# Kernel tuning notes

Hardware: AMD Instinct MI355X
Metric: run time of the kernel (lower is better)

## Reference

```python
import jax, jax.numpy as jnp
import numpy as np

D_MODEL = 1024
N_HEADS = 16
WINDOW = 256
S_DIM = 128
BATCH = 1
SEQ = 4096
EPS = 1e-5


def setup_inputs() -> dict:
    key = jax.random.key(0)
    ks = jax.random.split(key, 10)
    d, s = D_MODEL, S_DIM

    def w(k, shape, fan_in):
        return jax.random.normal(k, shape, jnp.float32) * (fan_in ** -0.5)

    return {
        "x": jax.random.normal(ks[0], (BATCH, SEQ, d), jnp.float32),
        "ln1_g": jnp.ones((d,), jnp.float32), "ln1_b": jnp.zeros((d,), jnp.float32),
        "ln2_g": jnp.ones((d,), jnp.float32), "ln2_b": jnp.zeros((d,), jnp.float32),
        "W_qkv": w(ks[1], (d, 3 * d), d),
        "W_O": w(ks[2], (d, d), d), "b_O": jnp.zeros((d,), jnp.float32),
        "W_ug": w(ks[3], (d, s + d), d), "b_ug": jnp.zeros((s + d,), jnp.float32),
        "B_w": w(ks[4], (d, s), d),
        "A": jax.random.uniform(ks[5], (s,), jnp.float32, -0.1, 0.1),
        "C_w": w(ks[6], (s, d), s),
        "mlp_W1": w(ks[7], (d, 4 * d), d), "mlp_b1": jnp.zeros((4 * d,), jnp.float32),
        "mlp_W2": w(ks[8], (4 * d, d), 4 * d), "mlp_b2": jnp.zeros((d,), jnp.float32),
    }


def _layernorm(x, g, b):
    mu = jnp.mean(x, -1, keepdims=True)
    var = jnp.mean((x - mu) ** 2, -1, keepdims=True)
    return (x - mu) * jax.lax.rsqrt(var + EPS) * g + b


def _windowed_attn(xn, W_qkv, W_O, b_O):
    # Exact windowed causal attention: key j allowed iff j <= i and i - j < WINDOW.
    # Implemented block-locally (chunk size C = WINDOW) so no O(T^2) mask/scores
    # are materialized, matching the SDPA band-mask math exactly.
    Bq, T, d = xn.shape
    H, Dh, C = N_HEADS, d // N_HEADS, WINDOW
    N = T // C  # SEQ must be a multiple of WINDOW
    qkv = xn @ W_qkv
    q, k, v = jnp.split(qkv, 3, axis=-1)

    def blk(t):
        return t.reshape(Bq, T, H, Dh).transpose(0, 2, 1, 3).reshape(Bq, H, N, C, Dh)

    Qb, Kb, Vb = blk(q), blk(k), blk(v)

    def win(t):  # prepend previous block (zeros for block 0) -> [B,H,N,2C,Dh]
        prev = jnp.concatenate([jnp.zeros_like(t[:, :, :1]), t[:, :, :-1]], axis=2)
        return jnp.concatenate([prev, t], axis=3)

    Kw, Vw = win(Kb), win(Vb)
    scores = jnp.einsum('bhncd,bhnkd->bhnck', Qb, Kw) / np.sqrt(Dh).astype(np.float32)
    qi = jnp.arange(C)[:, None]
    kk = jnp.arange(2 * C)[None, :]
    band = (kk > qi) & (kk <= qi + C)            # window band within 2C keys
    mask = jnp.where((jnp.arange(N) == 0)[:, None, None], band & (kk >= C), band)
    scores = jnp.where(mask[None, None], scores, -jnp.inf)
    p = jax.nn.softmax(scores, axis=-1)
    o = jnp.einsum('bhnck,bhnkd->bhncd', p, Vw)
    o = o.reshape(Bq, H, T, Dh).transpose(0, 2, 1, 3).reshape(Bq, T, d)
    return o @ W_O + b_O


def reference(x, ln1_g, ln1_b, ln2_g, ln2_b, W_qkv, W_O, b_O, W_ug, b_ug,
              B_w, A, C_w, mlp_W1, mlp_b1, mlp_W2, mlp_b2):
    xn = _layernorm(x, ln1_g, ln1_b)
    # local path: windowed causal attention (eval mode: dropout = identity)
    attn = _windowed_attn(xn, W_qkv, W_O, b_O)
    # global path: linear SSM  s_t = A * s_{t-1} + (B x_t + u_t),  y_t = C s_t
    ug = xn @ W_ug + b_ug
    u = ug[..., :S_DIM]
    g = jax.nn.sigmoid(ug[..., S_DIM:])          # learnable fusion gate, [B,T,d]
    drive = xn @ B_w + u                          # [B,T,S]

    def step(s, ut):
        s2 = A * s + ut
        return s2, s2

    s0 = jnp.zeros((x.shape[0], S_DIM), x.dtype)
    _, states = jax.lax.scan(step, s0, drive.transpose(1, 0, 2))  # [T,B,S]
    y_ssm = jnp.einsum('tbs,sd->btd', states, C_w)
    # gated fusion + residual
    x = x + g * attn + (1.0 - g) * y_ssm
    # MLP block (exact GELU, as nn.GELU default)
    h = _layernorm(x, ln2_g, ln2_b)
    x = x + jax.nn.gelu(h @ mlp_W1 + mlp_b1, approximate=False) @ mlp_W2 + mlp_b2
    return x
```

## Files before the change

### kernel.cpp

```cpp
#include <hip/hip_runtime.h>
#include <hip/hip_bf16.h>
#include <math.h>

typedef short bf16x8 __attribute__((ext_vector_type(8)));
typedef float f32x4  __attribute__((ext_vector_type(4)));

#define GLOBAL_AS __attribute__((address_space(1)))
#define LDS_AS    __attribute__((address_space(3)))

__device__ __forceinline__ void async16(const void* g, void* l) {
  __builtin_amdgcn_global_load_lds((GLOBAL_AS void*)(g), (LDS_AS void*)(l), 16, 0, 0);
}

__device__ __forceinline__ unsigned short f2bf(float f){
  union { float f; unsigned u; } x; x.f = f;
  return (unsigned short)((x.u + 0x7fffu + ((x.u >> 16) & 1u)) >> 16);
}
__device__ __forceinline__ float bf2f(short s){
  union { unsigned u; float f; } x; x.u = ((unsigned)(unsigned short)s) << 16;
  return x.f;
}
__device__ __forceinline__ float gelu_f(float x){
  return 0.5f*x*(1.f+erff(x*0.70710678118654752f));
}

__global__ __launch_bounds__(256) void ln_bf16(const float* __restrict__ in,
    const float* __restrict__ gg, const float* __restrict__ bb, short* __restrict__ out)
{
  const int row = blockIdx.x;
  const int tid = threadIdx.x;
  const float4 v = reinterpret_cast<const float4*>(in + (size_t)row*1024)[tid];
  float s  = v.x+v.y+v.z+v.w;
  float sq = v.x*v.x+v.y*v.y+v.z*v.z+v.w*v.w;
  #pragma unroll
  for (int off=32; off; off>>=1){ s += __shfl_xor(s,off); sq += __shfl_xor(sq,off); }
  __shared__ float ss[4], qs[4];
  const int wid = tid>>6, lane = tid&63;
  if (lane==0){ ss[wid]=s; qs[wid]=sq; }
  __syncthreads();
  s  = ss[0]+ss[1]+ss[2]+ss[3];
  sq = qs[0]+qs[1]+qs[2]+qs[3];
  const float mu  = s * (1.f/1024.f);
  const float var = sq*(1.f/1024.f) - mu*mu;
  const float rs  = rsqrtf(var + 1e-5f);
  const float4 g4 = reinterpret_cast<const float4*>(gg)[tid];
  const float4 b4 = reinterpret_cast<const float4*>(bb)[tid];
  ushort4 o;
  o.x = f2bf((v.x-mu)*rs*g4.x+b4.x);
  o.y = f2bf((v.y-mu)*rs*g4.y+b4.y);
  o.z = f2bf((v.z-mu)*rs*g4.z+b4.z);
  o.w = f2bf((v.w-mu)*rs*g4.w+b4.w);
  *reinterpret_cast<ushort4*>(out + (size_t)row*1024 + tid*4) = o;
}

__device__ __forceinline__ void conv_body(const float* __restrict__ in,
    short* __restrict__ out, int K, int N, const float* __restrict__ add, int addN,
    int bx, int by)
{
  __shared__ float tile[32][33];
  const int n0 = bx*32, k0 = by*32;
  const int r = threadIdx.x >> 3, c4 = (threadIdx.x & 7)*4;
  float4 v = *reinterpret_cast<const float4*>(&in[(size_t)(k0+r)*N + n0 + c4]);
  if (add && (n0 + c4) < addN) {
    const float* ap = &add[(size_t)(k0+r)*addN + n0 + c4];
    v.x += ap[0]; v.y += ap[1]; v.z += ap[2]; v.w += ap[3];
  }
  tile[r][c4+0]=v.x; tile[r][c4+1]=v.y; tile[r][c4+2]=v.z; tile[r][c4+3]=v.w;
  __syncthreads();
  ushort4 o;
  o.x = f2bf(tile[c4+0][r]); o.y = f2bf(tile[c4+1][r]);
  o.z = f2bf(tile[c4+2][r]); o.w = f2bf(tile[c4+3][r]);
  *reinterpret_cast<ushort4*>(&out[(size_t)(n0+r)*K + k0 + c4]) = o;
}

__global__ __launch_bounds__(256) void prep_weights(
    const float* __restrict__ W_qkv, const float* __restrict__ W_O,
    const float* __restrict__ W_ug,  const float* __restrict__ B_w,
    const float* __restrict__ C_w,   const float* __restrict__ W1,
    const float* __restrict__ W2,
    short* __restrict__ wT_qkv, short* __restrict__ wT_o,
    short* __restrict__ wT_ug,  short* __restrict__ wT_c,
    short* __restrict__ wT_1,   short* __restrict__ wT_2)
{
  const int bid = blockIdx.x;
  if (bid < 3072) {
    conv_body(W_qkv, wT_qkv, 1024, 3072, nullptr, 0, bid % 96, bid / 96);
  } else if (bid < 4224) {
    const int j = bid - 3072;
    conv_body(W_ug, wT_ug, 1024, 1152, B_w, 128, j % 36, j / 36);
  } else if (bid < 5248) {
    const int j = bid - 4224;
    conv_body(W_O, wT_o, 1024, 1024, nullptr, 0, j % 32, j / 32);
  } else if (bid < 5376) {
    const int j = bid - 5248;
    conv_body(C_w, wT_c, 128, 1024, nullptr, 0, j % 32, j / 32);
  } else if (bid < 9472) {
    const int j = bid - 5376;
    conv_body(W1, wT_1, 1024, 4096, nullptr, 0, j % 128, j / 128);
  } else {
    const int j = bid - 9472;
    conv_body(W2, wT_2, 4096, 1024, nullptr, 0, j % 32, j / 32);
  }
}

template<int EPI>
__global__ __launch_bounds__(512) void gemm256(
    const short* __restrict__ A, const short* __restrict__ Bt,
    const float* __restrict__ bias, short* __restrict__ Cout,
    int M, int N, int K)
{
  extern __shared__ char lds[];
  const int tid = threadIdx.x;
  const int ln = tid & 63, w = tid >> 6;
  const int wr = w >> 2, wc = w & 3;
  const int lane15 = ln & 15, lgrp = ln >> 4;

  const int gx = gridDim.x;
  const int nwg = gx * gridDim.y;
  int id = blockIdx.y * gx + blockIdx.x;
  if ((nwg & 7) == 0) { const int cpx = nwg >> 3; id = (id & 7) * cpx + (id >> 3); }
  const int m0 = (id / gx) * 256, n0 = (id % gx) * 256;

  const int NT = K >> 6;

  f32x4 acc[8][4];
  #pragma unroll
  for (int i=0;i<8;i++)
    #pragma unroll
    for (int j=0;j<4;j++) acc[i][j] = (f32x4){0.f,0.f,0.f,0.f};

  #define STG256(k0_, bufA_, bufB_, p_) { \
    const int slot = (p_)*512 + tid; \
    const int row = slot >> 3, blk = slot & 7; \
    const int sblk = blk ^ (row & 7); \
    async16(A  + (size_t)(m0+row)*K + (k0_) + sblk*8, (bufA_) + slot*16); \
    async16(Bt + (size_t)(n0+row)*K + (k0_) + sblk*8, (bufB_) + slot*16); }

  {
    char* bA = lds, *bB = lds + 32768;
    STG256(0, bA, bB, 0); STG256(0, bA, bB, 1); STG256(0, bA, bB, 2); STG256(0, bA, bB, 3);
    if (NT > 1) { char* cA = lds + 65536, *cB = cA + 32768; STG256(64, cA, cB, 0); }
    asm volatile("s_waitcnt vmcnt(0)" ::: "memory");
    __builtin_amdgcn_s_barrier();
    __builtin_amdgcn_sched_barrier(0);
  }

  for (int kt = 0; kt < NT; ++kt) {
    const int cur = kt & 1;
    char* rdA = lds + cur*65536;  char* rdB = rdA + 32768;
    char* wrA = lds + (cur^1)*65536; char* wrB = wrA + 32768;
    const int kn = (kt+1) << 6;
    bf16x8 bfr[4][2];
    #pragma unroll
    for (int ni = 0; ni < 4; ni++) {
      const int row = wc*64 + ni*16 + lane15;
      #pragma unroll
      for (int ks = 0; ks < 2; ks++) {
        const int b = (ks*4 + lgrp) ^ (row & 7);
        bfr[ni][ks] = *reinterpret_cast<const bf16x8*>(rdB + (row*8 + b)*16);
      }
    }
    if (kt+1 < NT) STG256(kn, wrA, wrB, 1);
    #pragma unroll
    for (int mq = 0; mq < 2; ++mq) {
      bf16x8 af[4][2];
      #pragma unroll
      for (int mi = 0; mi < 4; mi++) {
        const int row = wr*128 + (mq*4+mi)*16 + lane15;
        #pragma unroll
        for (int ks = 0; ks < 2; ks++) {
          const int b = (ks*4 + lgrp) ^ (row & 7);
          af[mi][ks] = *reinterpret_cast<const bf16x8*>(rdA + (row*8 + b)*16);
        }
      }
      if (kt+1 < NT) STG256(kn, wrA, wrB, 2+mq);
      #pragma unroll
      for (int mi = 0; mi < 4; mi++)
        #pragma unroll
        for (int ni = 0; ni < 4; ni++)
          #pragma unroll
          for (int ks = 0; ks < 2; ks++)
            acc[mq*4+mi][ni] = __builtin_amdgcn_mfma_f32_16x16x32_bf16(
                af[mi][ks], bfr[ni][ks], acc[mq*4+mi][ni], 0, 0, 0);
    }
    if (kt+1 < NT) {
      __builtin_amdgcn_s_barrier();
      if (kt+2 < NT) {
        STG256((kt+2) << 6, rdA, rdB, 0);
        asm volatile("s_waitcnt vmcnt(2)" ::: "memory");
      } else {
        asm volatile("s_waitcnt vmcnt(0)" ::: "memory");
      }
      __builtin_amdgcn_s_barrier();
      __builtin_amdgcn_sched_barrier(0);
    }
  }
  #undef STG256

  #pragma unroll
  for (int ni = 0; ni < 4; ni++) {
    const int col = n0 + wc*64 + ni*16 + lane15;
    const float bv = bias ? bias[col] : 0.f;
    #pragma unroll
    for (int mi = 0; mi < 8; mi++) {
      #pragma unroll
      for (int r = 0; r < 4; r++) {
        const int row = m0 + wr*128 + mi*16 + lgrp*4 + r;
        float v = acc[mi][ni][r] + bv;
        Cout[(size_t)row*N + col] = (short)f2bf(v);
      }
    }
  }
}

template<int MT, int EPI>
__global__ __launch_bounds__(256) void gemm128(
    const short* __restrict__ A, const short* __restrict__ Bt,
    const float* __restrict__ bias,
    short* __restrict__ e_g,
    void* __restrict__ Cout, int M, int N, int K)
{
  constexpr int BM  = MT * 32;
  constexpr int ABY = BM * 128;
  constexpr int STR = ABY + 16384;
  constexpr int MPQ = MT / 2;
  extern __shared__ char lds[];
  const int tid = threadIdx.x;
  const int ln = tid & 63, w = tid >> 6;
  const int wr = w >> 1, wc = w & 1;
  const int lane15 = ln & 15, lgrp = ln >> 4;

  const int gx = gridDim.x;
  const int nwg = gx * gridDim.y;
  int id = blockIdx.y * gx + blockIdx.x;
  if ((nwg & 7) == 0) { const int cpx = nwg >> 3; id = (id & 7) * cpx + (id >> 3); }
  const int m0 = (id / gx) * BM, n0 = (id % gx) * 128;

  const int NT = K >> 6;

  f32x4 acc[MT][4];
  #pragma unroll
  for (int i=0;i<MT;i++)
    #pragma unroll
    for (int j=0;j<4;j++) acc[i][j] = (f32x4){0.f,0.f,0.f,0.f};

  #define STG(k0_, bufA_, bufB_, p_) { \
    const int slot = (p_)*256 + tid; \
    const int row = slot >> 3, blk = slot & 7; \
    const int sblk = blk ^ (row & 7); \
    if ((p_) < MT) async16(A + (size_t)(m0+row)*K + (k0_) + sblk*8, (bufA_) + slot*16); \
    async16(Bt + (size_t)(n0+row)*K + (k0_) + sblk*8, (bufB_) + slot*16); }

  {
    char* bA = lds, *bB = lds + ABY;
    STG(0, bA, bB, 0); STG(0, bA, bB, 1); STG(0, bA, bB, 2); STG(0, bA, bB, 3);
    if (NT > 1) { char* cA = lds + STR, *cB = cA + ABY; STG(64, cA, cB, 0); }
    asm volatile("s_waitcnt vmcnt(0)" ::: "memory");
    __builtin_amdgcn_s_barrier();
    __builtin_amdgcn_sched_barrier(0);
  }

  for (int kt = 0; kt < NT; ++kt) {
    const int cur = kt & 1;
    char* rdA = lds + cur*STR;   char* rdB = rdA + ABY;
    char* wrA = lds + (cur^1)*STR; char* wrB = wrA + ABY;
    const int kn = (kt+1) << 6;
    bf16x8 bfr[4][2];
    #pragma unroll
    for (int ni = 0; ni < 4; ni++) {
      const int row = wc*64 + ni*16 + lane15;
      #pragma unroll
      for (int ks = 0; ks < 2; ks++) {
        const int b = (ks*4 + lgrp) ^ (row & 7);
        bfr[ni][ks] = *reinterpret_cast<const bf16x8*>(rdB + (row*8 + b)*16);
      }
    }
    if (kt+1 < NT) STG(kn, wrA, wrB, 1);
    #pragma unroll
    for (int mq = 0; mq < 2; ++mq) {
      bf16x8 af[MPQ][2];
      #pragma unroll
      for (int mi = 0; mi < MPQ; mi++) {
        const int row = wr*(MT*16) + (mq*MPQ+mi)*16 + lane15;
        #pragma unroll
        for (int ks = 0; ks < 2; ks++) {
          const int b = (ks*4 + lgrp) ^ (row & 7);
          af[mi][ks] = *reinterpret_cast<const bf16x8*>(rdA + (row*8 + b)*16);
        }
      }
      if (kt+1 < NT) STG(kn, wrA, wrB, 2+mq);
      #pragma unroll
      for (int mi = 0; mi < MPQ; mi++)
        #pragma unroll
        for (int ni = 0; ni < 4; ni++)
          #pragma unroll
          for (int ks = 0; ks < 2; ks++)
            acc[mq*MPQ+mi][ni] = __builtin_amdgcn_mfma_f32_16x16x32_bf16(
                af[mi][ks], bfr[ni][ks], acc[mq*MPQ+mi][ni], 0, 0, 0);
    }
    if (kt+1 < NT) {
      __builtin_amdgcn_s_barrier();
      if (kt+2 < NT) {
        STG((kt+2) << 6, rdA, rdB, 0);
        asm volatile("s_waitcnt vmcnt(2)" ::: "memory");
      } else {
        asm volatile("s_waitcnt vmcnt(0)" ::: "memory");
      }
      __builtin_amdgcn_s_barrier();
      __builtin_amdgcn_sched_barrier(0);
    }
  }
  #undef STG

  #pragma unroll
  for (int ni = 0; ni < 4; ni++) {
    const int col = n0 + wc*64 + ni*16 + lane15;
    const float bv = bias ? bias[col] : 0.f;
    #pragma unroll
    for (int mi = 0; mi < MT; mi++) {
      #pragma unroll
      for (int r = 0; r < 4; r++) {
        const int row = m0 + wr*(MT*16) + mi*16 + lgrp*4 + r;
        float v = acc[mi][ni][r] + bv;
        if (EPI == 1) {
          if (col < 128) ((float*)Cout)[(size_t)row*128 + col] = v;
          else {
            const float gs = 1.f/(1.f+__expf(-v));
            e_g[(size_t)row*1024 + col - 128] = (short)f2bf(gs);
          }
        } else if (EPI == 2) {
          ((short*)Cout)[(size_t)row*N + col] = (short)f2bf(gelu_f(v));
        } else {
          float* o = (float*)Cout;
          o[(size_t)row*N + col] = v + o[(size_t)row*N + col];
        }
      }
    }
  }
}

__global__ __launch_bounds__(256) void wo_comb(
    const short* __restrict__ A1, const short* __restrict__ B1t,
    const short* __restrict__ A2, const short* __restrict__ B2t,
    const float* __restrict__ bias, const float* __restrict__ e_x,
    const short* __restrict__ e_g, float* __restrict__ Cout)
{
  constexpr int ABY = 8192;
  constexpr int STR = ABY + 16384;
  extern __shared__ char lds[];
  const int tid = threadIdx.x;
  const int ln = tid & 63, w = tid >> 6;
  const int wr = w >> 1, wc = w & 1;
  const int lane15 = ln & 15, lgrp = ln >> 4;
  const int K = 1024, N = 1024;

  const int gx = gridDim.x;
  const int nwg = gx * gridDim.y;
  int id = blockIdx.y * gx + blockIdx.x;
  if ((nwg & 7) == 0) { const int cpx = nwg >> 3; id = (id & 7) * cpx + (id >> 3); }
  const int m0 = (id / gx) * 64, n0 = (id % gx) * 128;

  f32x4 acc1[2][4], acc2[2][4];
  #pragma unroll
  for (int i=0;i<2;i++)
    #pragma unroll
    for (int j=0;j<4;j++){ acc1[i][j] = (f32x4){0.f,0.f,0.f,0.f}; acc2[i][j] = (f32x4){0.f,0.f,0.f,0.f}; }

  #define STGW(Asrc_, Bsrc_, AK_, k0_, bufA_, bufB_, p_) { \
    const int slot = (p_)*256 + tid; \
    const int row = slot >> 3, blk = slot & 7; \
    const int sblk = blk ^ (row & 7); \
    if ((p_) < 2) async16(Asrc_ + (size_t)(m0+row)*(AK_) + (k0_) + sblk*8, (bufA_) + slot*16); \
    async16(Bsrc_ + (size_t)(n0+row)*(AK_) + (k0_) + sblk*8, (bufB_) + slot*16); }

  {
    char* bA = lds, *bB = lds + ABY;
    STGW(A1, B1t, K, 0, bA, bB, 0); STGW(A1, B1t, K, 0, bA, bB, 1);
    STGW(A1, B1t, K, 0, bA, bB, 2); STGW(A1, B1t, K, 0, bA, bB, 3);
    { char* cA = lds + STR, *cB = cA + ABY; STGW(A1, B1t, K, 64, cA, cB, 0); }
    asm volatile("s_waitcnt vmcnt(0)" ::: "memory");
    __builtin_amdgcn_s_barrier();
    __builtin_amdgcn_sched_barrier(0);
  }

  const int NT = 16;
  for (int kt = 0; kt < NT; ++kt) {
    const int cur = kt & 1;
    char* rdA = lds + cur*STR;   char* rdB = rdA + ABY;
    char* wrA = lds + (cur^1)*STR; char* wrB = wrA + ABY;
    const int kn = (kt+1) << 6;
    bf16x8 bfr[4][2];
    #pragma unroll
    for (int ni = 0; ni < 4; ni++) {
      const int row = wc*64 + ni*16 + lane15;
      #pragma unroll
      for (int ks = 0; ks < 2; ks++) {
        const int b = (ks*4 + lgrp) ^ (row & 7);
        bfr[ni][ks] = *reinterpret_cast<const bf16x8*>(rdB + (row*8 + b)*16);
      }
    }
    if (kt+1 < NT) STGW(A1, B1t, K, kn, wrA, wrB, 1);
    #pragma unroll
    for (int mq = 0; mq < 2; ++mq) {
      bf16x8 af[2];
      {
        const int row = wr*32 + mq*16 + lane15;
        #pragma unroll
        for (int ks = 0; ks < 2; ks++) {
          const int b = (ks*4 + lgrp) ^ (row & 7);
          af[ks] = *reinterpret_cast<const bf16x8*>(rdA + (row*8 + b)*16);
        }
      }
      if (kt+1 < NT) STGW(A1, B1t, K, kn, wrA, wrB, 2+mq);
      #pragma unroll
      for (int ni = 0; ni < 4; ni++)
        #pragma unroll
        for (int ks = 0; ks < 2; ks++)
          acc1[mq][ni] = __builtin_amdgcn_mfma_f32_16x16x32_bf16(
              af[ks], bfr[ni][ks], acc1[mq][ni], 0, 0, 0);
    }
    if (kt+1 < NT) {
      __builtin_amdgcn_s_barrier();
      if (kt+2 < NT) {
        STGW(A1, B1t, K, (kt+2) << 6, rdA, rdB, 0);
        asm volatile("s_waitcnt vmcnt(2)" ::: "memory");
      } else {
        asm volatile("s_waitcnt vmcnt(0)" ::: "memory");
      }
      __builtin_amdgcn_s_barrier();
      __builtin_amdgcn_sched_barrier(0);
    }
  }

  __builtin_amdgcn_s_barrier();
  {
    char* bA0 = lds,       *bB0 = lds + ABY;
    char* bA1 = lds + STR, *bB1 = bA1 + ABY;
    STGW(A2, B2t, 128, 0,  bA0, bB0, 0); STGW(A2, B2t, 128, 0,  bA0, bB0, 1);
    STGW(A2, B2t, 128, 0,  bA0, bB0, 2); STGW(A2, B2t, 128, 0,  bA0, bB0, 3);
    STGW(A2, B2t, 128, 64, bA1, bB1, 0); STGW(A2, B2t, 128, 64, bA1, bB1, 1);
    STGW(A2, B2t, 128, 64, bA1, bB1, 2); STGW(A2, B2t, 128, 64, bA1, bB1, 3);
    asm volatile("s_waitcnt vmcnt(0)" ::: "memory");
    __builtin_amdgcn_s_barrier();
  }
  #pragma unroll
  for (int t2 = 0; t2 < 2; ++t2) {
    char* rdA = lds + t2*STR; char* rdB = rdA + ABY;
    bf16x8 bfr2[4][2];
    #pragma unroll
    for (int ni = 0; ni < 4; ni++) {
      const int brow = wc*64 + ni*16 + lane15;
      #pragma unroll
      for (int ks = 0; ks < 2; ks++) {
        const int b = (ks*4 + lgrp) ^ (brow & 7);
        bfr2[ni][ks] = *reinterpret_cast<const bf16x8*>(rdB + (brow*8 + b)*16);
      }
    }
    #pragma unroll
    for (int mi = 0; mi < 2; mi++) {
      bf16x8 af[2];
      const int row = wr*32 + mi*16 + lane15;
      #pragma unroll
      for (int ks = 0; ks < 2; ks++) {
        const int b = (ks*4 + lgrp) ^ (row & 7);
        af[ks] = *reinterpret_cast<const bf16x8*>(rdA + (row*8 + b)*16);
      }
      #pragma unroll
      for (int ni = 0; ni < 4; ni++)
        #pragma unroll
        for (int ks = 0; ks < 2; ks++)
          acc2[mi][ni] = __builtin_amdgcn_mfma_f32_16x16x32_bf16(af[ks], bfr2[ni][ks], acc2[mi][ni], 0, 0, 0);
    }
  }
  #undef STGW

  #pragma unroll
  for (int ni = 0; ni < 4; ni++) {
    const int col = n0 + wc*64 + ni*16 + lane15;
    const float bv = bias[col];
    #pragma unroll
    for (int mi = 0; mi < 2; mi++) {
      #pragma unroll
      for (int r = 0; r < 4; r++) {
        const int row = m0 + wr*32 + mi*16 + lgrp*4 + r;
        const float g = bf2f(e_g[(size_t)row*1024 + col]);
        Cout[(size_t)row*N + col] = e_x[(size_t)row*1024 + col]
            + g*(acc1[mi][ni][r] + bv) + (1.f-g)*acc2[mi][ni][r];
      }
    }
  }
}

#define ATS 72
__global__ __launch_bounds__(256) void attn_mfma(const short* __restrict__ qkv,
                                                 short* __restrict__ attn_out)
{
  __shared__ short Qs[64*ATS];
  __shared__ short Ks[64*ATS];
  __shared__ short Vt[64*ATS];
  __shared__ short Ps[4][16*ATS];
  const int tid = threadIdx.x;
  const int ln = tid & 63, w = tid >> 6;
  const int qt0 = (blockIdx.x >> 4) * 64;
  const int h = blockIdx.x & 15;

  {
    const int jr = tid >> 3, d0 = (tid & 7) * 8;
    #pragma unroll
    for (int p = 0; p < 2; p++) {
      const int j = jr + p*32;
      const bf16x8 v = *reinterpret_cast<const bf16x8*>(&qkv[(size_t)(qt0 + j)*3072 + h*64 + d0]);
      const int blk = (d0 >> 3) ^ (j & 7);
      *reinterpret_cast<bf16x8*>(&Qs[j*ATS + blk*8]) = v;
    }
  }

  float mrow[4], lrow[4];
  f32x4 oacc[4];
  #pragma unroll
  for (int r=0;r<4;r++){ mrow[r] = -1e30f; lrow[r] = 0.f; }
  #pragma unroll
  for (int df=0;df<4;df++) oacc[df] = (f32x4){0.f,0.f,0.f,0.f};

  const int qrow_lane = w*16 + (ln>>4)*4;
  const int qtile = qt0 >> 6;
  const int cstart = (qtile >= 4) ? 0 : (4 - qtile);

  for (int c = cstart; c < 5; c++) {
    const int cs = qt0 - 256 + c*64;
    {
      const int jr = tid >> 3, d0 = (tid & 7) * 8;
      #pragma unroll
      for (int p = 0; p < 2; p++) {
        const int j = jr + p*32;
        const size_t krow = (size_t)(cs + j)*3072 + h*64;
        const bf16x8 kv = *reinterpret_cast<const bf16x8*>(&qkv[krow + 1024 + d0]);
        const int blk = (d0>>3) ^ (j & 7);
        *reinterpret_cast<bf16x8*>(&Ks[j*ATS + blk*8]) = kv;
        const bf16x8 vv = *reinterpret_cast<const bf16x8*>(&qkv[krow + 2048 + d0]);
        #pragma unroll
        for (int i = 0; i < 8; i++) {
          const int d = d0 + i;
          const int jb = (j >> 3) ^ ((d >> 3) & 7);
          Vt[d*ATS + jb*8 + (j & 7)] = ((const short*)&vv)[i];
        }
      }
    }
    __syncthreads();

    bf16x8 aq[2];
    #pragma unroll
    for (int ks=0; ks<2; ks++){
      const int row = w*16 + (ln & 15);
      const int b = (ks*4 + (ln>>4)) ^ (row & 7);
      aq[ks] = *reinterpret_cast<const bf16x8*>(&Qs[row*ATS + b*8]);
    }
    float sv[4][4];
    #pragma unroll
    for (int nf=0; nf<4; nf++){
      const int krow = nf*16 + (ln & 15);
      f32x4 s = (f32x4){0.f,0.f,0.f,0.f};
      #pragma unroll
      for (int ks=0; ks<2; ks++){
        const int b = (ks*4 + (ln>>4)) ^ (krow & 7);
        const bf16x8 bk = *reinterpret_cast<const bf16x8*>(&Ks[krow*ATS + b*8]);
        s = __builtin_amdgcn_mfma_f32_16x16x32_bf16(aq[ks], bk, s, 0, 0, 0);
      }
      const int k_abs = cs + nf*16 + (ln & 15);
      #pragma unroll
      for (int r=0;r<4;r++){
        const int t_abs = qt0 + qrow_lane + r;
        const bool valid = (k_abs <= t_abs) && (k_abs >= t_abs - 255);
        sv[nf][r] = valid ? s[r]*0.125f : -1e30f;
      }
    }
    float cm[4], alpha[4], rs[4];
    #pragma unroll
    for (int r=0;r<4;r++){
      cm[r] = fmaxf(fmaxf(sv[0][r],sv[1][r]), fmaxf(sv[2][r],sv[3][r]));
      #pragma unroll
      for (int off=1; off<16; off<<=1) cm[r] = fmaxf(cm[r], __shfl_xor(cm[r], off));
      const float mnew = fmaxf(mrow[r], cm[r]);
      alpha[r] = __expf(mrow[r] - mnew);
      mrow[r] = mnew;
      rs[r] = 0.f;
    }
    #pragma unroll
    for (int nf=0; nf<4; nf++){
      const int pcol = nf*16 + (ln & 15);
      #pragma unroll
      for (int r=0;r<4;r++){
        const float p = (sv[nf][r] <= -1e29f) ? 0.f : __expf(sv[nf][r] - mrow[r]);
        rs[r] += p;
        const int prow = (ln>>4)*4 + r;
        const int pb = (pcol>>3) ^ (prow & 7);
        Ps[w][prow*ATS + pb*8 + (pcol & 7)] = (short)f2bf(p);
      }
    }
    #pragma unroll
    for (int r=0;r<4;r++){
      #pragma unroll
      for (int off=1; off<16; off<<=1) rs[r] += __shfl_xor(rs[r], off);
      lrow[r] = lrow[r]*alpha[r] + rs[r];
      #pragma unroll
      for (int df=0; df<4; df++) oacc[df][r] *= alpha[r];
    }
    bf16x8 ap[2];
    #pragma unroll
    for (int ks=0; ks<2; ks++){
      const int prow = (ln & 15);
      const int b = (ks*4 + (ln>>4)) ^ (prow & 7);
      ap[ks] = *reinterpret_cast<const bf16x8*>(&Ps[w][prow*ATS + b*8]);
    }
    #pragma unroll
    for (int df=0; df<4; df++){
      const int vrow = df*16 + (ln & 15);
      #pragma unroll
      for (int ks=0; ks<2; ks++){
        const int b = (ks*4 + (ln>>4)) ^ ((vrow>>3) & 7);
        const bf16x8 bv = *reinterpret_cast<const bf16x8*>(&Vt[vrow*ATS + b*8]);
        oacc[df] = __builtin_amdgcn_mfma_f32_16x16x32_bf16(ap[ks], bv, oacc[df], 0, 0, 0);
      }
    }
    __syncthreads();
  }

  #pragma unroll
  for (int df=0; df<4; df++)
    #pragma unroll
    for (int r=0; r<4; r++){
      const int t = qt0 + qrow_lane + r;
      const int d = df*16 + (ln & 15);
      attn_out[(size_t)t*1024 + h*64 + d] = (short)f2bf(oacc[df][r] / lrow[r]);
    }
}

__global__ __launch_bounds__(256) void scan_kernel(const float* __restrict__ drive,
    const float* __restrict__ Aa, short* __restrict__ states)
{
  const int idx = blockIdx.x*256 + threadIdx.x;
  const int t = idx >> 7, s = idx & 127;
  const float a = Aa[s];
  float acc = 0.f, pw = 1.f;
  const int kmax = (t+1 < 16) ? (t+1) : 16;
  for (int k=0;k<kmax;k++){
    acc = fmaf(pw, drive[(size_t)(t-k)*128 + s], acc);
    pw *= a;
  }
  states[idx] = (short)f2bf(acc);
}

extern "C" void kernel_launch(void* const* d_in, const int* in_sizes, int n_in,
                              void* d_out, int out_size, void* d_ws, size_t ws_size,
                              hipStream_t stream)
{
  const float* x     = (const float*)d_in[0];
  const float* ln1_g = (const float*)d_in[1];
  const float* ln1_b = (const float*)d_in[2];
  const float* ln2_g = (const float*)d_in[3];
  const float* ln2_b = (const float*)d_in[4];
  const float* W_qkv = (const float*)d_in[5];
  const float* W_O   = (const float*)d_in[6];
  const float* b_O   = (const float*)d_in[7];
  const float* W_ug  = (const float*)d_in[8];
  const float* b_ug  = (const float*)d_in[9];
  const float* B_w   = (const float*)d_in[10];
  const float* A     = (const float*)d_in[11];
  const float* C_w   = (const float*)d_in[12];
  const float* W1    = (const float*)d_in[13];
  const float* b1    = (const float*)d_in[14];
  const float* W2    = (const float*)d_in[15];
  const float* b2    = (const float*)d_in[16];
  float* out = (float*)d_out;
  char* ws = (char*)d_ws;

  short* qkv_bf = (short*)(ws + 0);
  short* attn_bf= (short*)(ws + 25165824);
  short* xn_bf  = (short*)(ws + 33554432);
  short* g_bf   = (short*)(ws + 41943040);
  float* drive  = (float*)(ws + 50331648);
  short* st_bf  = (short*)(ws + 52428800);
  short* wT_qkv = (short*)(ws + 53542912);
  short* wT_o   = (short*)(ws + 59834368);
  short* wT_ug  = (short*)(ws + 61931520);
  short* wT_c   = (short*)(ws + 64290816);
  short* wT_1   = (short*)(ws + 64552960);
  short* wT_2   = (short*)(ws + 72941568);
  short* mid_bf = (short*)(ws + 0);
  short* h_bf   = xn_bf;

  static bool attr_done = false;
  if (!attr_done) {
    hipFuncSetAttribute((const void*)gemm256<0>, hipFuncAttributeMaxDynamicSharedMemorySize, 131072);
    hipFuncSetAttribute((const void*)(gemm128<4,2>), hipFuncAttributeMaxDynamicSharedMemorySize, 65536);
    hipFuncSetAttribute((const void*)(gemm128<2,1>), hipFuncAttributeMaxDynamicSharedMemorySize, 49152);
    hipFuncSetAttribute((const void*)(gemm128<2,3>), hipFuncAttributeMaxDynamicSharedMemorySize, 49152);
    hipFuncSetAttribute((const void*)wo_comb, hipFuncAttributeMaxDynamicSharedMemorySize, 49152);
    attr_done = true;
  }

  prep_weights<<<13568, 256, 0, stream>>>(W_qkv, W_O, W_ug, B_w, C_w, W1, W2,
                                          wT_qkv, wT_o, wT_ug, wT_c, wT_1, wT_2);

  ln_bf16<<<4096, 256, 0, stream>>>(x, ln1_g, ln1_b, xn_bf);
  gemm256<0><<<dim3(12,16), 512, 131072, stream>>>(xn_bf, wT_qkv, nullptr, qkv_bf, 4096, 3072, 1024);
  attn_mfma<<<1024, 256, 0, stream>>>(qkv_bf, attn_bf);
  gemm128<2,1><<<dim3(9,64), 256, 49152, stream>>>(xn_bf, wT_ug, b_ug, g_bf, drive, 4096, 1152, 1024);
  scan_kernel<<<2048, 256, 0, stream>>>(drive, A, st_bf);
  wo_comb<<<dim3(8,64), 256, 49152, stream>>>(attn_bf, wT_o, st_bf, wT_c, b_O, x, g_bf, out);
  ln_bf16<<<4096, 256, 0, stream>>>(out, ln2_g, ln2_b, h_bf);
  gemm128<4,2><<<dim3(32,32), 256, 65536, stream>>>(h_bf, wT_1, b1, nullptr, mid_bf, 4096, 4096, 1024);
  gemm128<2,3><<<dim3(8,64), 256, 49152, stream>>>(mid_bf, wT_2, b2, nullptr, out, 4096, 1024, 4096);
}
```

Measured before the change: 249.6 us.

## Use 256-tile GEMM for MLP up-projection and pre-transpose V for async attention loads

The MLP first GEMM moves from the 128-row tile kernel to the larger 256x256 tile kernel, with GELU applied in a new epilogue variant. Attention now reads V from a pre-transposed global buffer written by a new transpose kernel. K, Q and V tiles load straight into LDS with async global-to-LDS copies, replacing the per-element register-to-LDS transposed stores. This trades an extra kernel launch and an extra V round trip through memory for cheaper LDS staging and higher GEMM data reuse.

```diff
diff --git a/kernel.cpp b/kernel.cpp
--- a/kernel.cpp
+++ b/kernel.cpp
@@ -103,6 +103,21 @@
   }
 }
 
+__global__ __launch_bounds__(256) void vt_pre(const short* __restrict__ qkv,
+                                              short* __restrict__ vtg)
+{
+  __shared__ short tile[32][36];
+  const int t0 = (blockIdx.x & 127) * 32;
+  const int r0 = (blockIdx.x >> 7) * 32;
+  const int r = threadIdx.x >> 3, c4 = (threadIdx.x & 7) * 4;
+  const short* src = qkv + (size_t)(t0 + r)*3072 + 2048 + r0 + c4;
+  *reinterpret_cast<short4*>(&tile[r][c4]) = *reinterpret_cast<const short4*>(src);
+  __syncthreads();
+  short4 o;
+  o.x = tile[c4+0][r]; o.y = tile[c4+1][r]; o.z = tile[c4+2][r]; o.w = tile[c4+3][r];
+  *reinterpret_cast<short4*>(&vtg[(size_t)(r0 + r)*4096 + t0 + c4]) = o;
+}
+
 template<int EPI>
 __global__ __launch_bounds__(512) void gemm256(
     const short* __restrict__ A, const short* __restrict__ Bt,
@@ -207,6 +222,7 @@
       for (int r = 0; r < 4; r++) {
         const int row = m0 + wr*128 + mi*16 + lgrp*4 + r;
         float v = acc[mi][ni][r] + bv;
+        if (EPI == 1) v = gelu_f(v);
         Cout[(size_t)row*N + col] = (short)f2bf(v);
       }
     }
@@ -328,8 +344,6 @@
             const float gs = 1.f/(1.f+__expf(-v));
             e_g[(size_t)row*1024 + col - 128] = (short)f2bf(gs);
           }
-        } else if (EPI == 2) {
-          ((short*)Cout)[(size_t)row*N + col] = (short)f2bf(gelu_f(v));
         } else {
           float* o = (float*)Cout;
           o[(size_t)row*N + col] = v + o[(size_t)row*N + col];
@@ -491,28 +505,25 @@
   }
 }
 
-#define ATS 72
 __global__ __launch_bounds__(256) void attn_mfma(const short* __restrict__ qkv,
-                                                 short* __restrict__ attn_out)
-{
-  __shared__ short Qs[64*ATS];
-  __shared__ short Ks[64*ATS];
-  __shared__ short Vt[64*ATS];
-  __shared__ short Ps[4][16*ATS];
+    const short* __restrict__ vtg, short* __restrict__ attn_out)
+{
+  __shared__ short Qs[64*64];
+  __shared__ short Ks[64*64];
+  __shared__ short Vs[64*64];
+  __shared__ short Ps[4][16*64];
   const int tid = threadIdx.x;
   const int ln = tid & 63, w = tid >> 6;
+  const int lane15 = ln & 15, lgrp = ln >> 4;
   const int qt0 = (blockIdx.x >> 4) * 64;
   const int h = blockIdx.x & 15;
 
-  {
-    const int jr = tid >> 3, d0 = (tid & 7) * 8;
-    #pragma unroll
-    for (int p = 0; p < 2; p++) {
-      const int j = jr + p*32;
-      const bf16x8 v = *reinterpret_cast<const bf16x8*>(&qkv[(size_t)(qt0 + j)*3072 + h*64 + d0]);
-      const int blk = (d0 >> 3) ^ (j & 7);
-      *reinterpret_cast<bf16x8*>(&Qs[j*ATS + blk*8]) = v;
-    }
+  #pragma unroll
+  for (int l = 0; l < 2; l++) {
+    const int slot = l*256 + tid;
+    const int row = slot >> 3, blk = slot & 7;
+    const int sblk = blk ^ (row & 7);
+    async16(qkv + (size_t)(qt0+row)*3072 + h*64 + sblk*8, (char*)Qs + slot*16);
   }
 
   float mrow[4], lrow[4];
@@ -522,51 +533,42 @@
   #pragma unroll
   for (int df=0;df<4;df++) oacc[df] = (f32x4){0.f,0.f,0.f,0.f};
 
-  const int qrow_lane = w*16 + (ln>>4)*4;
+  const int qrow_lane = w*16 + lgrp*4;
   const int qtile = qt0 >> 6;
   const int cstart = (qtile >= 4) ? 0 : (4 - qtile);
 
   for (int c = cstart; c < 5; c++) {
     const int cs = qt0 - 256 + c*64;
-    {
-      const int jr = tid >> 3, d0 = (tid & 7) * 8;
-      #pragma unroll
-      for (int p = 0; p < 2; p++) {
-        const int j = jr + p*32;
-        const size_t krow = (size_t)(cs + j)*3072 + h*64;
-        const bf16x8 kv = *reinterpret_cast<const bf16x8*>(&qkv[krow + 1024 + d0]);
-        const int blk = (d0>>3) ^ (j & 7);
-        *reinterpret_cast<bf16x8*>(&Ks[j*ATS + blk*8]) = kv;
-        const bf16x8 vv = *reinterpret_cast<const bf16x8*>(&qkv[krow + 2048 + d0]);
-        #pragma unroll
-        for (int i = 0; i < 8; i++) {
-          const int d = d0 + i;
-          const int jb = (j >> 3) ^ ((d >> 3) & 7);
-          Vt[d*ATS + jb*8 + (j & 7)] = ((const short*)&vv)[i];
-        }
-      }
-    }
+    #pragma unroll
+    for (int l = 0; l < 2; l++) {
+      const int slot = l*256 + tid;
+      const int row = slot >> 3, blk = slot & 7;
+      const int sblk = blk ^ (row & 7);
+      async16(qkv + (size_t)(cs+row)*3072 + 1024 + h*64 + sblk*8, (char*)Ks + slot*16);
+      async16(vtg + (size_t)(h*64+row)*4096 + cs + sblk*8, (char*)Vs + slot*16);
+    }
+    asm volatile("s_waitcnt vmcnt(0)" ::: "memory");
     __syncthreads();
 
     bf16x8 aq[2];
     #pragma unroll
     for (int ks=0; ks<2; ks++){
-      const int row = w*16 + (ln & 15);
-      const int b = (ks*4 + (ln>>4)) ^ (row & 7);
-      aq[ks] = *reinterpret_cast<const bf16x8*>(&Qs[row*ATS + b*8]);
+      const int row = w*16 + lane15;
+      const int b = (ks*4 + lgrp) ^ (row & 7);
+      aq[ks] = *reinterpret_cast<const bf16x8*>((char*)Qs + (row*8 + b)*16);
     }
     float sv[4][4];
     #pragma unroll
     for (int nf=0; nf<4; nf++){
-      const int krow = nf*16 + (ln & 15);
+      const int krow = nf*16 + lane15;
       f32x4 s = (f32x4){0.f,0.f,0.f,0.f};
       #pragma unroll
       for (int ks=0; ks<2; ks++){
-        const int b = (ks*4 + (ln>>4)) ^ (krow & 7);
-        const bf16x8 bk = *reinterpret_cast<const bf16x8*>(&Ks[krow*ATS + b*8]);
+        const int b = (ks*4 + lgrp) ^ (krow & 7);
+        const bf16x8 bk = *reinterpret_cast<const bf16x8*>((char*)Ks + (krow*8 + b)*16);
         s = __builtin_amdgcn_mfma_f32_16x16x32_bf16(aq[ks], bk, s, 0, 0, 0);
       }
-      const int k_abs = cs + nf*16 + (ln & 15);
+      const int k_abs = cs + nf*16 + lane15;
       #pragma unroll
       for (int r=0;r<4;r++){
         const int t_abs = qt0 + qrow_lane + r;
@@ -587,14 +589,14 @@
     }
     #pragma unroll
     for (int nf=0; nf<4; nf++){
-      const int pcol = nf*16 + (ln & 15);
+      const int pcol = nf*16 + lane15;
       #pragma unroll
       for (int r=0;r<4;r++){
         const float p = (sv[nf][r] <= -1e29f) ? 0.f : __expf(sv[nf][r] - mrow[r]);
         rs[r] += p;
-        const int prow = (ln>>4)*4 + r;
+        const int prow = lgrp*4 + r;
         const int pb = (pcol>>3) ^ (prow & 7);
-        Ps[w][prow*ATS + pb*8 + (pcol & 7)] = (short)f2bf(p);
+        Ps[w][prow*64 + pb*8 + (pcol & 7)] = (short)f2bf(p);
       }
     }
     #pragma unroll
@@ -608,17 +610,17 @@
     bf16x8 ap[2];
     #pragma unroll
     for (int ks=0; ks<2; ks++){
-      const int prow = (ln & 15);
-      const int b = (ks*4 + (ln>>4)) ^ (prow & 7);
-      ap[ks] = *reinterpret_cast<const bf16x8*>(&Ps[w][prow*ATS + b*8]);
+      const int prow = lane15;
+      const int b = (ks*4 + lgrp) ^ (prow & 7);
+      ap[ks] = *reinterpret_cast<const bf16x8*>((char*)(Ps[w]) + (prow*8 + b)*16);
     }
     #pragma unroll
     for (int df=0; df<4; df++){
-      const int vrow = df*16 + (ln & 15);
+      const int vrow = df*16 + lane15;
       #pragma unroll
       for (int ks=0; ks<2; ks++){
-        const int b = (ks*4 + (ln>>4)) ^ ((vrow>>3) & 7);
-        const bf16x8 bv = *reinterpret_cast<const bf16x8*>(&Vt[vrow*ATS + b*8]);
+        const int b = (ks*4 + lgrp) ^ (vrow & 7);
+        const bf16x8 bv = *reinterpret_cast<const bf16x8*>((char*)Vs + (vrow*8 + b)*16);
         oacc[df] = __builtin_amdgcn_mfma_f32_16x16x32_bf16(ap[ks], bv, oacc[df], 0, 0, 0);
       }
     }
@@ -630,7 +632,7 @@
     #pragma unroll
     for (int r=0; r<4; r++){
       const int t = qt0 + qrow_lane + r;
-      const int d = df*16 + (ln & 15);
+      const int d = df*16 + lane15;
       attn_out[(size_t)t*1024 + h*64 + d] = (short)f2bf(oacc[df][r] / lrow[r]);
     }
 }
@@ -686,13 +688,14 @@
   short* wT_c   = (short*)(ws + 64290816);
   short* wT_1   = (short*)(ws + 64552960);
   short* wT_2   = (short*)(ws + 72941568);
+  short* vtg    = (short*)(ws + 81330176);
   short* mid_bf = (short*)(ws + 0);
   short* h_bf   = xn_bf;
 
   static bool attr_done = false;
   if (!attr_done) {
     hipFuncSetAttribute((const void*)gemm256<0>, hipFuncAttributeMaxDynamicSharedMemorySize, 131072);
-    hipFuncSetAttribute((const void*)(gemm128<4,2>), hipFuncAttributeMaxDynamicSharedMemorySize, 65536);
+    hipFuncSetAttribute((const void*)gemm256<1>, hipFuncAttributeMaxDynamicSharedMemorySize, 131072);
     hipFuncSetAttribute((const void*)(gemm128<2,1>), hipFuncAttributeMaxDynamicSharedMemorySize, 49152);
     hipFuncSetAttribute((const void*)(gemm128<2,3>), hipFuncAttributeMaxDynamicSharedMemorySize, 49152);
     hipFuncSetAttribute((const void*)wo_comb, hipFuncAttributeMaxDynamicSharedMemorySize, 49152);
@@ -704,11 +707,12 @@
 
   ln_bf16<<<4096, 256, 0, stream>>>(x, ln1_g, ln1_b, xn_bf);
   gemm256<0><<<dim3(12,16), 512, 131072, stream>>>(xn_bf, wT_qkv, nullptr, qkv_bf, 4096, 3072, 1024);
-  attn_mfma<<<1024, 256, 0, stream>>>(qkv_bf, attn_bf);
+  vt_pre<<<4096, 256, 0, stream>>>(qkv_bf, vtg);
+  attn_mfma<<<1024, 256, 0, stream>>>(qkv_bf, vtg, attn_bf);
   gemm128<2,1><<<dim3(9,64), 256, 49152, stream>>>(xn_bf, wT_ug, b_ug, g_bf, drive, 4096, 1152, 1024);
   scan_kernel<<<2048, 256, 0, stream>>>(drive, A, st_bf);
   wo_comb<<<dim3(8,64), 256, 49152, stream>>>(attn_bf, wT_o, st_bf, wT_c, b_O, x, g_bf, out);
   ln_bf16<<<4096, 256, 0, stream>>>(out, ln2_g, ln2_b, h_bf);
-  gemm128<4,2><<<dim3(32,32), 256, 65536, stream>>>(h_bf, wT_1, b1, nullptr, mid_bf, 4096, 4096, 1024);
+  gemm256<1><<<dim3(16,16), 512, 131072, stream>>>(h_bf, wT_1, b1, mid_bf, 4096, 4096, 1024);
   gemm128<2,3><<<dim3(8,64), 256, 49152, stream>>>(mid_bf, wT_2, b2, nullptr, out, 4096, 1024, 4096);
 }
```

Result: faster. 243.5 us (-2.4%).
